# Kernel tuning notes

Hardware: AMD Instinct MI355X
Metric: run time of the kernel (lower is better)

The kernel has to match this reference:

```python
import jax, jax.numpy as jnp
import numpy as np

E = 2          # e_layers
DM = 64        # d_model == emb_dim (hardcoded 64 in out_layer)
H = 8          # n_heads
DH = DM // H
DFF = 256      # d_ff
P = 16         # patch_size
STRIDE = P // 2
SL = 4096      # seq_len
NPATCH = (SL - P) // STRIDE + 1   # 511
PRED = 96
B, M = 8, 8
FACTOR = 5
EPS = 1e-5


def setup_inputs() -> dict:
    key = jax.random.key(0)
    ks = jax.random.split(key, 32)
    s = jnp.float32(0.02)
    f = lambda i, shape: jax.random.normal(ks[i], shape, jnp.float32)
    d = {
        "x_enc": f(0, (B, SL, M)),
        "x_mark_enc": f(1, (B, SL, 4)),
        "x_dec": f(2, (B, PRED, M)),
        "x_mark_dec": f(3, (B, PRED, 4)),
        # patch embedding  Linear(patch_size -> emb_dim)
        "in_W": f(4, (DM, P)) * s,
        "in_b": jnp.zeros((DM,), jnp.float32),
        # per-layer attention projections (stacked over e_layers)
        "Wq": f(5, (E, DM, DM)) * s, "bq": jnp.zeros((E, DM), jnp.float32),
        "Wk": f(6, (E, DM, DM)) * s, "bk": jnp.zeros((E, DM), jnp.float32),
        "Wv": f(7, (E, DM, DM)) * s, "bv": jnp.zeros((E, DM), jnp.float32),
        "Wo": f(8, (E, DM, DM)) * s, "bo": jnp.zeros((E, DM), jnp.float32),
        # FFN (Conv1d kernel=1 == Linear)
        "c1_W": f(9, (E, DFF, DM)) * s, "c1_b": jnp.zeros((E, DFF), jnp.float32),
        "c2_W": f(10, (E, DM, DFF)) * s, "c2_b": jnp.zeros((E, DM), jnp.float32),
        # layer norms
        "ln1_g": jnp.ones((E, DM), jnp.float32), "ln1_b": jnp.zeros((E, DM), jnp.float32),
        "ln2_g": jnp.ones((E, DM), jnp.float32), "ln2_b": jnp.zeros((E, DM), jnp.float32),
        "lnf_g": jnp.ones((DM,), jnp.float32), "lnf_b": jnp.zeros((DM,), jnp.float32),
        # decode head  Linear(64*num_patches -> pred_len)
        "out_W": f(11, (PRED, DM * NPATCH)) * s,
        "out_b": jnp.zeros((PRED,), jnp.float32),
    }
    return d


def _ln(x, g, b):
    mu = x.mean(-1, keepdims=True)
    var = ((x - mu) ** 2).mean(-1, keepdims=True)
    return (x - mu) * jax.lax.rsqrt(var + EPS) * g + b


def _prob_attn(q, k, v, key):
    # q,k,v: [Bn, H, L, Dh]  (ProbSparse attention, mask_flag=False)
    Bn, h, Lq, Dh = q.shape
    Lk = k.shape[2]
    U_part = min(int(FACTOR * np.ceil(np.log(Lk))), Lk)   # sampled keys per query
    u = min(int(FACTOR * np.ceil(np.log(Lq))), Lq)        # top-u active queries
    idx = jax.random.randint(key, (Lq, U_part), 0, Lk)
    k_sample = k[:, :, idx, :]                             # [Bn,H,Lq,U,Dh]
    qk_sample = jnp.einsum('bhld,bhlud->bhlu', q, k_sample)
    # sparsity measure: max - sum/L_K (as in torch code)
    sparsity = qk_sample.max(-1) - qk_sample.sum(-1) / jnp.float32(Lk)
    _, top_idx = jax.lax.top_k(sparsity, u)                # [Bn,H,u]
    q_red = jnp.take_along_axis(q, top_idx[..., None], axis=2)  # [Bn,H,u,Dh]
    scale = jax.lax.rsqrt(jnp.float32(Dh))
    scores = jnp.einsum('bhud,bhkd->bhuk', q_red, k) * scale    # [Bn,H,u,Lk]
    attn = jax.nn.softmax(scores, axis=-1)
    # lazy context: mean of V for inactive queries, attn@V for active ones
    ctx = jnp.broadcast_to(v.mean(axis=2, keepdims=True), q.shape)
    upd = jnp.einsum('bhuk,bhkd->bhud', attn, v)
    bi = jnp.arange(Bn)[:, None, None]
    hi = jnp.arange(h)[None, :, None]
    ctx = ctx.at[bi, hi, top_idx].set(upd)
    return ctx.transpose(0, 2, 1, 3)  # [Bn,L,H,Dh]


def reference(x_enc, x_mark_enc, x_dec, x_mark_dec, in_W, in_b, Wq, bq, Wk, bk,
              Wv, bv, Wo, bo, c1_W, c1_b, c2_W, c2_b, ln1_g, ln1_b, ln2_g, ln2_b,
              lnf_g, lnf_b, out_W, out_b):
    Bb, L, Mm = x_enc.shape
    x = x_enc.transpose(0, 2, 1)  # b l m -> b m l
    pidx = jnp.arange(NPATCH)[:, None] * STRIDE + jnp.arange(P)[None, :]
    patches = x[:, :, pidx]                         # [B,M,N,P] (unfold)
    z = patches.reshape(Bb * Mm, NPATCH, P) @ in_W.T + in_b  # [BM,N,DM]
    akey = jax.random.key(1)
    for e in range(E):
        q = (z @ Wq[e].T + bq[e]).reshape(Bb * Mm, NPATCH, H, DH).transpose(0, 2, 1, 3)
        k = (z @ Wk[e].T + bk[e]).reshape(Bb * Mm, NPATCH, H, DH).transpose(0, 2, 1, 3)
        v = (z @ Wv[e].T + bv[e]).reshape(Bb * Mm, NPATCH, H, DH).transpose(0, 2, 1, 3)
        ctx = _prob_attn(q, k, v, jax.random.fold_in(akey, e))
        new_x = ctx.reshape(Bb * Mm, NPATCH, DM) @ Wo[e].T + bo[e]
        x1 = _ln(z + new_x, ln1_g[e], ln1_b[e])
        y = jax.nn.gelu(x1 @ c1_W[e].T + c1_b[e], approximate=False)
        y = y @ c2_W[e].T + c2_b[e]
        z = _ln(x1 + y, ln2_g[e], ln2_b[e])
    z = _ln(z, lnf_g, lnf_b)
    out = z.reshape(Bb * Mm, -1) @ out_W.T + out_b   # [BM, pred_len]
    out = out.reshape(Bb, Mm, PRED).transpose(0, 2, 1)  # (b m) l -> b l m
    return out[:, -PRED:, :]
```

## Files before the change

kernel.cpp:

```cpp
#include <hip/hip_runtime.h>
#include <hip/hip_bf16.h>
#include <stdint.h>
#include <math.h>

typedef __hip_bfloat16 bf16;
typedef __attribute__((ext_vector_type(8))) short short8;
typedef __attribute__((ext_vector_type(4))) short short4v;
typedef __attribute__((ext_vector_type(4))) float fx4;

#define NP 511
#define UPART 35
#define NTOK 32704
#define NBITS 17885
#define LN_EPS 1e-5f

__host__ __device__ __forceinline__ void tf2x32(uint32_t k0, uint32_t k1,
                                                uint32_t x0, uint32_t x1,
                                                uint32_t* o0, uint32_t* o1) {
  uint32_t ks2 = k0 ^ k1 ^ 0x1BD11BDAu;
  x0 += k0; x1 += k1;
#define TFR(r) { x0 += x1; x1 = (x1 << (r)) | (x1 >> (32 - (r))); x1 ^= x0; }
  TFR(13) TFR(15) TFR(26) TFR(6)   x0 += k1;  x1 += ks2 + 1u;
  TFR(17) TFR(29) TFR(16) TFR(24)  x0 += ks2; x1 += k0 + 2u;
  TFR(13) TFR(15) TFR(26) TFR(6)   x0 += k0;  x1 += k1 + 3u;
  TFR(17) TFR(29) TFR(16) TFR(24)  x0 += k1;  x1 += ks2 + 4u;
  TFR(13) TFR(15) TFR(26) TFR(6)   x0 += ks2; x1 += k0 + 5u;
#undef TFR
  *o0 = x0; *o1 = x1;
}

__device__ __forceinline__ float ldin(const void* p, int i, int f32) {
  if (f32) return ((const float*)p)[i];
  return __bfloat162float(((const bf16*)p)[i]);
}
__device__ __forceinline__ unsigned short f2bf(float v) {
  uint32_t u = __builtin_bit_cast(uint32_t, v);
  u += 0x7fffu + ((u >> 16) & 1u);
  return (unsigned short)(u >> 16);
}
__device__ __forceinline__ float bfb2f(uint32_t h) {
  uint32_t u = h << 16;
  return __builtin_bit_cast(float, u);
}
__device__ __forceinline__ float lo16(uint32_t w) { return bfb2f(w & 0xFFFFu); }
__device__ __forceinline__ float hi16(uint32_t w) { return bfb2f(w >> 16); }
__device__ __forceinline__ uint32_t pack2(float a, float b) {
  return (uint32_t)f2bf(a) | ((uint32_t)f2bf(b) << 16);
}
__device__ __forceinline__ int lanes_below(unsigned long long m) {
  return __builtin_amdgcn_mbcnt_hi((uint32_t)(m >> 32),
         __builtin_amdgcn_mbcnt_lo((uint32_t)m, 0));
}

__global__ void zero_out_kernel(bf16* __restrict__ out, int n) {
  int i = blockIdx.x * 256 + threadIdx.x;
  if (i < n) out[i] = __float2bfloat16(0.f);
}

__global__ void gen_idx_kernel(int* __restrict__ idxT,
    uint32_t ka0, uint32_t ka1, uint32_t kb0, uint32_t kb1,
    const uint32_t* __restrict__ lnfg, int* __restrict__ flag) {
  if (blockIdx.x == 0 && threadIdx.x == 0)
    flag[0] = (lnfg[0] == 0x3F800000u) ? 1 : 0;
  int i = blockIdx.x * 256 + threadIdx.x;
  if (i >= 2 * NBITS) return;
  int e = i / NBITS;
  uint32_t j = (uint32_t)(i - e * NBITS);
  uint32_t k0 = e ? kb0 : ka0, k1 = e ? kb1 : ka1;
  uint32_t o0, o1;
  tf2x32(k0, k1, 0u, j, &o0, &o1);
  uint32_t bits = o1;
  uint32_t hi = bits >> 16, lo = bits & 0xFFFFu;
  uint32_t off = ((hi % 511u) * 32u + (lo % 511u)) % 511u;
  int l = (int)(j / UPART), u = (int)(j % UPART);
  idxT[e * NBITS + u * NP + l] = (int)off;
}

__global__ __launch_bounds__(256) void embed_kernel(
    const void* __restrict__ xe, const void* __restrict__ inW,
    const void* __restrict__ inb, float* __restrict__ z,
    const int* __restrict__ flg) {
  __shared__ float xs[136 * 8];
  int f = flg[0];
  int b = blockIdx.x >> 5, nt = blockIdx.x & 31;
  int n0 = nt * 16;
  for (int i = threadIdx.x; i < 1088; i += 256) {
    int row = i >> 3, m = i & 7;
    int g = n0 * 8 + row;
    xs[i] = (g < 4096) ? ldin(xe, (b * 4096 + g) * 8 + m, f) : 0.f;
  }
  int d = threadIdx.x & 63, mg = threadIdx.x >> 6;
  float wreg[16];
#pragma unroll
  for (int p = 0; p < 16; ++p) wreg[p] = ldin(inW, d * 16 + p, f);
  float bd = ldin(inb, d, f);
  __syncthreads();
  for (int nl = 0; nl < 16; ++nl) {
    int n = n0 + nl;
    if (n >= NP) break;
#pragma unroll
    for (int mm = 0; mm < 2; ++mm) {
      int m = mg * 2 + mm;
      float acc = bd;
#pragma unroll
      for (int p = 0; p < 16; ++p)
        acc = fmaf(xs[(nl * 8 + p) * 8 + m], wreg[p], acc);
      int t = (b * 8 + m) * NP + n;
      z[(size_t)t * 64 + d] = acc;
    }
  }
}

__global__ __launch_bounds__(256) void qkv_kernel(
    const float* __restrict__ z,
    const void* __restrict__ Wq, const void* __restrict__ bq,
    const void* __restrict__ Wk, const void* __restrict__ bk,
    const void* __restrict__ Wv, const void* __restrict__ bv,
    bf16* __restrict__ qb, bf16* __restrict__ kb, bf16* __restrict__ vb,
    const int* __restrict__ flg, int e) {
  __shared__ short xb[64 * 72];
  __shared__ short wL[192 * 72];
  __shared__ float bqs[192];
  int f = flg[0];
  int t0 = blockIdx.x * 64;
  int tid = threadIdx.x;
  {
    const float4* xg = (const float4*)(z + (size_t)t0 * 64);
#pragma unroll
    for (int r = 0; r < 4; ++r) {
      int i4 = r * 256 + tid;
      float4 v = xg[i4];
      int t = (i4 * 4) >> 6, d = (i4 * 4) & 63;
      short4v h;
      h.x = (short)f2bf(v.x); h.y = (short)f2bf(v.y);
      h.z = (short)f2bf(v.z); h.w = (short)f2bf(v.w);
      *(short4v*)&xb[t * 72 + d] = h;
    }
  }
  if (!f) {
    const uint4* Wg0 = (const uint4*)((const bf16*)Wq + e * 4096);
    const uint4* Wg1 = (const uint4*)((const bf16*)Wk + e * 4096);
    const uint4* Wg2 = (const uint4*)((const bf16*)Wv + e * 4096);
#pragma unroll
    for (int r = 0; r < 2; ++r) {
      int i = r * 256 + tid;
      int row = i >> 3, c8 = (i & 7) * 8;
      *(uint4*)&wL[row * 72 + c8] = Wg0[i];
      *(uint4*)&wL[(64 + row) * 72 + c8] = Wg1[i];
      *(uint4*)&wL[(128 + row) * 72 + c8] = Wg2[i];
    }
  } else {
#pragma unroll
    for (int r = 0; r < 16; ++r) {
      int i = r * 256 + tid;
      int row = i >> 6, c = i & 63;
      wL[row * 72 + c] = (short)f2bf(((const float*)Wq)[e * 4096 + i]);
      wL[(64 + row) * 72 + c] = (short)f2bf(((const float*)Wk)[e * 4096 + i]);
      wL[(128 + row) * 72 + c] = (short)f2bf(((const float*)Wv)[e * 4096 + i]);
    }
  }
  if (tid < 192) {
    int t3 = tid >> 6, j = tid & 63;
    bqs[tid] = (t3 == 0) ? ldin(bq, e * 64 + j, f)
             : (t3 == 1) ? ldin(bk, e * 64 + j, f)
                         : ldin(bv, e * 64 + j, f);
  }
  __syncthreads();
  int lane = tid & 63, w = tid >> 6;
  int m0 = w * 16, col = lane & 15, quad = lane >> 4;
  short8 a0 = *(const short8*)&xb[(m0 + col) * 72 + quad * 8];
  short8 a1 = *(const short8*)&xb[(m0 + col) * 72 + 32 + quad * 8];
#pragma unroll
  for (int nt = 0; nt < 12; ++nt) {
    fx4 acc = {0.f, 0.f, 0.f, 0.f};
    short8 b0 = *(const short8*)&wL[(nt * 16 + col) * 72 + quad * 8];
    short8 b1 = *(const short8*)&wL[(nt * 16 + col) * 72 + 32 + quad * 8];
    acc = __builtin_amdgcn_mfma_f32_16x16x32_bf16(a0, b0, acc, 0, 0, 0);
    acc = __builtin_amdgcn_mfma_f32_16x16x32_bf16(a1, b1, acc, 0, 0, 0);
    int c = nt * 16 + col;
    int t3 = c >> 6, hd = c & 63, h = hd >> 3, d2 = hd & 7;
    bf16* base = (t3 == 0) ? qb : (t3 == 1) ? kb : vb;
    float bia = bqs[c];
#pragma unroll
    for (int reg = 0; reg < 4; ++reg) {
      int tok = t0 + m0 + quad * 4 + reg;
      int bm = tok / NP, n = tok - bm * NP;
      base[((size_t)(bm * 8 + h) * NP + n) * 8 + d2] =
          __float2bfloat16(acc[reg] + bia);
    }
  }
}

__global__ __launch_bounds__(512) void attn_fused_kernel(
    const bf16* __restrict__ qg, const bf16* __restrict__ kg,
    const bf16* __restrict__ vg, const int* __restrict__ idxT,
    bf16* __restrict__ ctx) {
  __shared__ uint32_t kkp[NP * 5 + 3];
  __shared__ uint32_t kvp[NP * 5 + 3];
  __shared__ float scF[8 * 512];
  __shared__ float spars[512];
  __shared__ float redv[256];
  __shared__ int topi[UPART];
  __shared__ float vmean[8];
  __shared__ unsigned char selflag[NP + 1];
  int bh = blockIdx.x;
  int bm = bh >> 3, h = bh & 7;
  size_t hb = (size_t)bh * NP * 8;
  int tid = threadIdx.x;
  int lane = tid & 63, wv = tid >> 6;
  {
    const uint4* k4 = (const uint4*)(kg + hb);
    const uint4* v4 = (const uint4*)(vg + hb);
    for (int n = tid; n < NP; n += 512) {
      uint4 b = k4[n], c = v4[n];
      uint32_t* dk = kkp + n * 5;
      uint32_t* dv = kvp + n * 5;
      dk[0] = b.x; dk[1] = b.y; dk[2] = b.z; dk[3] = b.w;
      dv[0] = c.x; dv[1] = c.y; dv[2] = c.z; dv[3] = c.w;
    }
  }
  __syncthreads();
  if (tid < NP) {
    int l = tid;
    uint4 a = ((const uint4*)(qg + hb))[l];
    float ql[8];
    ql[0] = lo16(a.x); ql[1] = hi16(a.x);
    ql[2] = lo16(a.y); ql[3] = hi16(a.y);
    ql[4] = lo16(a.z); ql[5] = hi16(a.z);
    ql[6] = lo16(a.w); ql[7] = hi16(a.w);
    float mxA = -1e30f, smA = 0.f, mxB = -1e30f, smB = 0.f;
#pragma unroll 6
    for (int u = 0; u < 18; ++u) {
      int j = idxT[u * NP + l];
      j = ((unsigned)j > 510u) ? 0 : j;
      const uint32_t* kr = kkp + j * 5;
      uint32_t w0 = kr[0], w1 = kr[1], w2 = kr[2], w3 = kr[3];
      float dt = 0.f;
      dt = fmaf(ql[0], lo16(w0), dt); dt = fmaf(ql[1], hi16(w0), dt);
      dt = fmaf(ql[2], lo16(w1), dt); dt = fmaf(ql[3], hi16(w1), dt);
      dt = fmaf(ql[4], lo16(w2), dt); dt = fmaf(ql[5], hi16(w2), dt);
      dt = fmaf(ql[6], lo16(w3), dt); dt = fmaf(ql[7], hi16(w3), dt);
      mxA = fmaxf(mxA, dt); smA += dt;
    }
#pragma unroll 6
    for (int u = 18; u < 35; ++u) {
      int j = idxT[u * NP + l];
      j = ((unsigned)j > 510u) ? 0 : j;
      const uint32_t* kr = kkp + j * 5;
      uint32_t w0 = kr[0], w1 = kr[1], w2 = kr[2], w3 = kr[3];
      float dt = 0.f;
      dt = fmaf(ql[0], lo16(w0), dt); dt = fmaf(ql[1], hi16(w0), dt);
      dt = fmaf(ql[2], lo16(w1), dt); dt = fmaf(ql[3], hi16(w1), dt);
      dt = fmaf(ql[4], lo16(w2), dt); dt = fmaf(ql[5], hi16(w2), dt);
      dt = fmaf(ql[6], lo16(w3), dt); dt = fmaf(ql[7], hi16(w3), dt);
      mxB = fmaxf(mxB, dt); smB += dt;
    }
    spars[l] = fmaxf(mxA, mxB) - (smA + smB) * (1.0f / 511.0f);
  }
  __syncthreads();
  if (tid < 64) {
    uint32_t key[8];
#pragma unroll
    for (int jj = 0; jj < 8; ++jj) {
      int ll = lane + jj * 64;
      if (ll < NP) {
        uint32_t u = __builtin_bit_cast(uint32_t, spars[ll]);
        key[jj] = (u & 0x80000000u) ? ~u : (u | 0x80000000u);
      } else key[jj] = 0u;
    }
    uint32_t p = 0u;
    for (int b = 31; b >= 0; --b) {
      uint32_t t = p | (1u << b);
      int cnt = 0;
#pragma unroll
      for (int jj = 0; jj < 8; ++jj)
        cnt += __popcll(__ballot(key[jj] >= t));
      if (cnt >= UPART) p = t;
    }
    int c1 = 0;
#pragma unroll
    for (int jj = 0; jj < 8; ++jj)
      c1 += __popcll(__ballot(key[jj] > p));
    int need = UPART - c1;
    int base = 0, taken = 0;
#pragma unroll
    for (int jj = 0; jj < 8; ++jj) {
      int ll = lane + jj * 64;
      bool gt = key[jj] > p;
      bool eq = key[jj] == p;
      unsigned long long meq = __ballot(eq);
      int beq = lanes_below(meq);
      bool sel = gt || (eq && (taken + beq) < need);
      unsigned long long msel = __ballot(sel);
      int pos = base + lanes_below(msel);
      if (sel) topi[pos] = ll;
      if (ll < NP) selflag[ll] = sel ? 1 : 0;
      base += __popcll(msel);
      taken += __popcll(meq);
    }
  } else if (tid >= 256) {
    int tt = tid - 256;
    int d = tt & 7, pt = tt >> 3;
    int c = d >> 1, odd = d & 1;
    float s = 0.f;
    for (int n = pt; n < NP; n += 32) {
      uint32_t w = kvp[n * 5 + c];
      s += odd ? hi16(w) : lo16(w);
    }
    redv[tt] = s;
  }
  __syncthreads();
  if (tid < 8) {
    float s = 0.f;
#pragma unroll
    for (int pt = 0; pt < 32; ++pt) s += redv[pt * 8 + tid];
    vmean[tid] = s * (1.0f / 511.0f);
  }
  __syncthreads();
  size_t cb = (size_t)bm * (NP * 64) + h * 8;
  if (tid < NP && !selflag[tid]) {
    uint4 pv;
    pv.x = pack2(vmean[0], vmean[1]);
    pv.y = pack2(vmean[2], vmean[3]);
    pv.z = pack2(vmean[4], vmean[5]);
    pv.w = pack2(vmean[6], vmean[7]);
    *(uint4*)(ctx + cb + (size_t)tid * 64) = pv;
  }
  const float scale = 0.35355339059327373f;
  float* myS = scF + wv * 512;
  int l0 = topi[wv];
  int l1 = topi[wv + 8];
  int l2 = topi[wv + 16];
  int l3 = topi[wv + 24];
  bool has5 = (wv + 32) < UPART;
  int l4 = has5 ? topi[wv + 32] : l0;
  l0 = ((unsigned)l0 > 510u) ? 0 : l0;
  l1 = ((unsigned)l1 > 510u) ? 0 : l1;
  l2 = ((unsigned)l2 > 510u) ? 0 : l2;
  l3 = ((unsigned)l3 > 510u) ? 0 : l3;
  l4 = ((unsigned)l4 > 510u) ? 0 : l4;
  const uint4* q4p = (const uint4*)(qg + hb);
  uint4 qv0 = q4p[l0];
  uint4 qv1 = q4p[l1];
  uint4 qv2 = q4p[l2];
  uint4 qv3 = q4p[l3];
  uint4 qv4 = q4p[l4];

  auto process = [&](uint4 a, int lsel) {
    float qs[8];
    qs[0] = lo16(a.x); qs[1] = hi16(a.x);
    qs[2] = lo16(a.y); qs[3] = hi16(a.y);
    qs[4] = lo16(a.z); qs[5] = hi16(a.z);
    qs[6] = lo16(a.w); qs[7] = hi16(a.w);
    float mx = -1e30f;
    for (int j = lane; j < NP; j += 64) {
      const uint32_t* kr = kkp + j * 5;
      uint32_t w0 = kr[0], w1 = kr[1], w2 = kr[2], w3 = kr[3];
      float d0 = qs[0] * lo16(w0);
      d0 = fmaf(qs[1], hi16(w0), d0);
      d0 = fmaf(qs[2], lo16(w1), d0);
      d0 = fmaf(qs[3], hi16(w1), d0);
      float d1 = qs[4] * lo16(w2);
      d1 = fmaf(qs[5], hi16(w2), d1);
      d1 = fmaf(qs[6], lo16(w3), d1);
      d1 = fmaf(qs[7], hi16(w3), d1);
      float sc = (d0 + d1) * scale;
      myS[j] = sc;
      mx = fmaxf(mx, sc);
    }
    for (int off = 32; off; off >>= 1) mx = fmaxf(mx, __shfl_xor(mx, off));
    float ssum = 0.f, acc[8];
#pragma unroll
    for (int d2 = 0; d2 < 8; ++d2) acc[d2] = 0.f;
    for (int j = lane; j < NP; j += 64) {
      float w = __expf(myS[j] - mx);
      ssum += w;
      const uint32_t* vr = kvp + j * 5;
      uint32_t x0 = vr[0], x1 = vr[1], x2 = vr[2], x3 = vr[3];
      acc[0] = fmaf(w, lo16(x0), acc[0]); acc[1] = fmaf(w, hi16(x0), acc[1]);
      acc[2] = fmaf(w, lo16(x1), acc[2]); acc[3] = fmaf(w, hi16(x1), acc[3]);
      acc[4] = fmaf(w, lo16(x2), acc[4]); acc[5] = fmaf(w, hi16(x2), acc[5]);
      acc[6] = fmaf(w, lo16(x3), acc[6]); acc[7] = fmaf(w, hi16(x3), acc[7]);
    }
    for (int off = 32; off; off >>= 1) {
      ssum += __shfl_xor(ssum, off);
#pragma unroll
      for (int d2 = 0; d2 < 8; ++d2) acc[d2] += __shfl_xor(acc[d2], off);
    }
    if (lane == 0) {
      float inv = 1.0f / ssum;
      uint4 pv;
      pv.x = pack2(acc[0] * inv, acc[1] * inv);
      pv.y = pack2(acc[2] * inv, acc[3] * inv);
      pv.z = pack2(acc[4] * inv, acc[5] * inv);
      pv.w = pack2(acc[6] * inv, acc[7] * inv);
      *(uint4*)(ctx + cb + (size_t)lsel * 64) = pv;
    }
  };
  process(qv0, l0);
  process(qv1, l1);
  process(qv2, l2);
  process(qv3, l3);
  if (has5) process(qv4, l4);
}

__global__ __launch_bounds__(256) void oproj_ln_kernel(
    const float* __restrict__ z, const bf16* __restrict__ ctx,
    const void* __restrict__ Wo, const void* __restrict__ bo,
    const void* __restrict__ g, const void* __restrict__ bb,
    float* __restrict__ x1, const int* __restrict__ flg, int e) {
  __shared__ short cbL[64 * 72];
  __shared__ short woL[64 * 72];
  __shared__ float zf[64 * 64];
  __shared__ float bos[64], gs[64], bbs[64];
  int f = flg[0];
  int t0 = blockIdx.x * 64;
  int tid = threadIdx.x;
  {
    const uint4* cg = (const uint4*)(ctx + (size_t)t0 * 64);
#pragma unroll
    for (int r = 0; r < 2; ++r) {
      int i = r * 256 + tid;
      uint4 v = cg[i];
      int row = i >> 3, c8 = (i & 7) * 8;
      *(uint4*)&cbL[row * 72 + c8] = v;
    }
    const float4* zg = (const float4*)(z + (size_t)t0 * 64);
#pragma unroll
    for (int r = 0; r < 4; ++r) {
      int i4 = r * 256 + tid;
      float4 v = zg[i4];
      int t = (i4 * 4) >> 6, d = (i4 * 4) & 63;
      *(float4*)&zf[t * 64 + d] = v;
    }
  }
  if (!f) {
    const uint4* Wg = (const uint4*)((const bf16*)Wo + e * 4096);
#pragma unroll
    for (int r = 0; r < 2; ++r) {
      int i = r * 256 + tid;
      int row = i >> 3, c8 = (i & 7) * 8;
      *(uint4*)&woL[row * 72 + c8] = Wg[i];
    }
  } else {
#pragma unroll
    for (int r = 0; r < 16; ++r) {
      int i = r * 256 + tid;
      int row = i >> 6, c = i & 63;
      woL[row * 72 + c] = (short)f2bf(((const float*)Wo)[e * 4096 + i]);
    }
  }
  if (tid < 64) {
    bos[tid] = ldin(bo, e * 64 + tid, f);
    gs[tid] = ldin(g, e * 64 + tid, f);
    bbs[tid] = ldin(bb, e * 64 + tid, f);
  }
  __syncthreads();
  int lane = tid & 63, w = tid >> 6;
  int m0 = w * 16, col = lane & 15, quad = lane >> 4;
  short8 a0 = *(const short8*)&cbL[(m0 + col) * 72 + quad * 8];
  short8 a1 = *(const short8*)&cbL[(m0 + col) * 72 + 32 + quad * 8];
  fx4 vacc[4];
#pragma unroll
  for (int nt = 0; nt < 4; ++nt) {
    fx4 acc = {0.f, 0.f, 0.f, 0.f};
    short8 b0 = *(const short8*)&woL[(nt * 16 + col) * 72 + quad * 8];
    short8 b1 = *(const short8*)&woL[(nt * 16 + col) * 72 + 32 + quad * 8];
    acc = __builtin_amdgcn_mfma_f32_16x16x32_bf16(a0, b0, acc, 0, 0, 0);
    acc = __builtin_amdgcn_mfma_f32_16x16x32_bf16(a1, b1, acc, 0, 0, 0);
    vacc[nt] = acc;
  }
  float vals[4][4];
  float ps[4], sq[4];
#pragma unroll
  for (int reg = 0; reg < 4; ++reg) { ps[reg] = 0.f; sq[reg] = 0.f; }
#pragma unroll
  for (int nt = 0; nt < 4; ++nt) {
    int d = nt * 16 + col;
#pragma unroll
    for (int reg = 0; reg < 4; ++reg) {
      int tl = m0 + quad * 4 + reg;
      float v = vacc[nt][reg] + bos[d] + zf[tl * 64 + d];
      vals[nt][reg] = v;
      ps[reg] += v; sq[reg] += v * v;
    }
  }
#pragma unroll
  for (int off = 1; off < 16; off <<= 1) {
#pragma unroll
    for (int reg = 0; reg < 4; ++reg) {
      ps[reg] += __shfl_xor(ps[reg], off);
      sq[reg] += __shfl_xor(sq[reg], off);
    }
  }
#pragma unroll
  for (int reg = 0; reg < 4; ++reg) {
    float mu = ps[reg] * (1.0f / 64.0f);
    float var = sq[reg] * (1.0f / 64.0f) - mu * mu;
    float rs = rsqrtf(fmaxf(var, 0.f) + LN_EPS);
    int tl = m0 + quad * 4 + reg;
#pragma unroll
    for (int nt = 0; nt < 4; ++nt) {
      int d = nt * 16 + col;
      x1[(size_t)(t0 + tl) * 64 + d] = (vals[nt][reg] - mu) * rs * gs[d] + bbs[d];
    }
  }
}

__global__ __launch_bounds__(256) void ffn_kernel(
    const float* __restrict__ x1,
    const void* __restrict__ W1, const void* __restrict__ b1,
    const void* __restrict__ W2, const void* __restrict__ b2,
    const void* __restrict__ g, const void* __restrict__ bb,
    float* __restrict__ zo, bf16* __restrict__ zfT,
    const void* __restrict__ lfg, const void* __restrict__ lfb,
    const int* __restrict__ flg, int e, int last) {
  __shared__ __align__(16) char smem[72960];
  short* wA  = (short*)smem;
  short* rB  = (short*)(smem + 36864);
  float* b1s = (float*)(smem + 70656);
  float* b2s = b1s + 256;
  float* gs  = b2s + 64;
  float* bbs = gs + 64;
  float* g2s = bbs + 64;
  float* bb2s = g2s + 64;
  int f = flg[0];
  int t0 = blockIdx.x * 64;
  int tid = threadIdx.x;
  {
    const float4* xg = (const float4*)(x1 + (size_t)t0 * 64);
#pragma unroll
    for (int r = 0; r < 4; ++r) {
      int i4 = r * 256 + tid;
      float4 v = xg[i4];
      int t = (i4 * 4) >> 6, d = (i4 * 4) & 63;
      short4v h;
      h.x = (short)f2bf(v.x); h.y = (short)f2bf(v.y);
      h.z = (short)f2bf(v.z); h.w = (short)f2bf(v.w);
      *(short4v*)&rB[t * 72 + d] = h;
    }
  }
  if (!f) {
    const uint4* W1g = (const uint4*)((const bf16*)W1 + e * 16384);
#pragma unroll
    for (int r = 0; r < 8; ++r) {
      int i = r * 256 + tid;
      uint4 v = W1g[i];
      int j = i >> 3, k = (i & 7) * 8;
      *(uint4*)&wA[j * 72 + k] = v;
    }
  } else {
    for (int r = 0; r < 64; ++r) {
      int i = r * 256 + tid;
      int j = i >> 6, k = i & 63;
      wA[j * 72 + k] = (short)f2bf(((const float*)W1)[e * 16384 + i]);
    }
  }
  b1s[tid] = ldin(b1, e * 256 + tid, f);
  if (tid < 64) {
    b2s[tid] = ldin(b2, e * 64 + tid, f);
    gs[tid] = ldin(g, e * 64 + tid, f);
    bbs[tid] = ldin(bb, e * 64 + tid, f);
    g2s[tid] = ldin(lfg, tid, f);
    bb2s[tid] = ldin(lfb, tid, f);
  }
  __syncthreads();

  int lane = tid & 63, w = tid >> 6;
  int m0 = w * 16;
  int col = lane & 15, quad = lane >> 4;
  short8 a0 = *(const short8*)&rB[(m0 + col) * 72 + quad * 8];
  short8 a1 = *(const short8*)&rB[(m0 + col) * 72 + 32 + quad * 8];
  __syncthreads();
#pragma unroll 4
  for (int nt = 0; nt < 16; ++nt) {
    fx4 acc = {0.f, 0.f, 0.f, 0.f};
    short8 bf0 = *(const short8*)&wA[(nt * 16 + col) * 72 + quad * 8];
    short8 bf1 = *(const short8*)&wA[(nt * 16 + col) * 72 + 32 + quad * 8];
    acc = __builtin_amdgcn_mfma_f32_16x16x32_bf16(a0, bf0, acc, 0, 0, 0);
    acc = __builtin_amdgcn_mfma_f32_16x16x32_bf16(a1, bf1, acc, 0, 0, 0);
    int j = nt * 16 + col;
    float bj = b1s[j];
#pragma unroll
    for (int reg = 0; reg < 4; ++reg) {
      float a = acc[reg] + bj;
      float ge = 0.5f * a * (1.0f + erff(a * 0.70710678118654752f));
      rB[(m0 + quad * 4 + reg) * 264 + j] = (short)f2bf(ge);
    }
  }
  __syncthreads();
  if (!f) {
    const uint4* W2g = (const uint4*)((const bf16*)W2 + e * 16384);
#pragma unroll
    for (int r = 0; r < 8; ++r) {
      int i = r * 256 + tid;
      uint4 v2 = W2g[i];
      int dd = i >> 5, c = (i & 31) * 8;
      *(uint4*)&wA[dd * 264 + c] = v2;
    }
  } else {
    for (int r = 0; r < 64; ++r) {
      int i = r * 256 + tid;
      int dd = i >> 8, c = i & 255;
      wA[dd * 264 + c] = (short)f2bf(((const float*)W2)[e * 16384 + i]);
    }
  }
  __syncthreads();
  short8 af[8];
#pragma unroll
  for (int kt = 0; kt < 8; ++kt)
    af[kt] = *(const short8*)&rB[(m0 + col) * 264 + kt * 32 + quad * 8];
  fx4 vacc[4];
#pragma unroll
  for (int nt = 0; nt < 4; ++nt) {
    fx4 acc = {0.f, 0.f, 0.f, 0.f};
#pragma unroll
    for (int kt = 0; kt < 8; ++kt) {
      short8 bfr = *(const short8*)&wA[(nt * 16 + col) * 264 + kt * 32 + quad * 8];
      acc = __builtin_amdgcn_mfma_f32_16x16x32_bf16(af[kt], bfr, acc, 0, 0, 0);
    }
    vacc[nt] = acc;
  }
  float vals[4][4];
  float ps[4], sq[4];
#pragma unroll
  for (int reg = 0; reg < 4; ++reg) { ps[reg] = 0.f; sq[reg] = 0.f; }
#pragma unroll
  for (int nt = 0; nt < 4; ++nt) {
    int d = nt * 16 + col;
#pragma unroll
    for (int reg = 0; reg < 4; ++reg) {
      int tl = m0 + quad * 4 + reg;
      float v = vacc[nt][reg] + b2s[d] + x1[(size_t)(t0 + tl) * 64 + d];
      vals[nt][reg] = v;
      ps[reg] += v; sq[reg] += v * v;
    }
  }
#pragma unroll
  for (int off = 1; off < 16; off <<= 1) {
#pragma unroll
    for (int reg = 0; reg < 4; ++reg) {
      ps[reg] += __shfl_xor(ps[reg], off);
      sq[reg] += __shfl_xor(sq[reg], off);
    }
  }
  if (!last) {
#pragma unroll
    for (int reg = 0; reg < 4; ++reg) {
      float mu = ps[reg] * (1.0f / 64.0f);
      float var = sq[reg] * (1.0f / 64.0f) - mu * mu;
      float rs = rsqrtf(fmaxf(var, 0.f) + LN_EPS);
      int tl = m0 + quad * 4 + reg;
#pragma unroll
      for (int nt = 0; nt < 4; ++nt) {
        int d = nt * 16 + col;
        zo[(size_t)(t0 + tl) * 64 + d] = (vals[nt][reg] - mu) * rs * gs[d] + bbs[d];
      }
    }
  } else {
    float ps2[4], sq2[4];
#pragma unroll
    for (int reg = 0; reg < 4; ++reg) { ps2[reg] = 0.f; sq2[reg] = 0.f; }
    float v2s[4][4];
#pragma unroll
    for (int reg = 0; reg < 4; ++reg) {
      float mu = ps[reg] * (1.0f / 64.0f);
      float var = sq[reg] * (1.0f / 64.0f) - mu * mu;
      float rs = rsqrtf(fmaxf(var, 0.f) + LN_EPS);
#pragma unroll
      for (int nt = 0; nt < 4; ++nt) {
        int d = nt * 16 + col;
        float v2 = (vals[nt][reg] - mu) * rs * gs[d] + bbs[d];
        v2s[nt][reg] = v2;
        ps2[reg] += v2; sq2[reg] += v2 * v2;
      }
    }
#pragma unroll
    for (int off = 1; off < 16; off <<= 1) {
#pragma unroll
      for (int reg = 0; reg < 4; ++reg) {
        ps2[reg] += __shfl_xor(ps2[reg], off);
        sq2[reg] += __shfl_xor(sq2[reg], off);
      }
    }
#pragma unroll
    for (int reg = 0; reg < 4; ++reg) {
      float mu = ps2[reg] * (1.0f / 64.0f);
      float var = sq2[reg] * (1.0f / 64.0f) - mu * mu;
      float rs = rsqrtf(fmaxf(var, 0.f) + LN_EPS);
      int tok = t0 + m0 + quad * 4 + reg;
      int bm = tok / NP, n = tok - bm * NP;
#pragma unroll
      for (int nt = 0; nt < 4; ++nt) {
        int d = nt * 16 + col;
        zfT[(size_t)n * 4096 + bm * 64 + d] =
            __float2bfloat16((v2s[nt][reg] - mu) * rs * g2s[d] + bb2s[d]);
      }
    }
  }
}

__global__ __launch_bounds__(256) void head1_kernel(
    const bf16* __restrict__ zfT, const void* __restrict__ W,
    float* __restrict__ partial, const int* __restrict__ flg) {
  __shared__ short aL[64 * 72];
  __shared__ short bL[96 * 72];
  int f = flg[0];
  int n = blockIdx.x;
  int tid = threadIdx.x;
  {
    const uint4* Ag = (const uint4*)(zfT + (size_t)n * 4096);
#pragma unroll
    for (int r = 0; r < 2; ++r) {
      int i = r * 256 + tid;
      uint4 v = Ag[i];
      int row = i >> 3, c = (i & 7) * 8;
      *(uint4*)&aL[row * 72 + c] = v;
    }
  }
  if (!f) {
    const uint4* Wg = (const uint4*)W;
#pragma unroll
    for (int r = 0; r < 3; ++r) {
      int i = r * 256 + tid;
      int p = i >> 3, c8 = i & 7;
      uint4 v = Wg[(size_t)p * 4088 + n * 8 + c8];
      *(uint4*)&bL[p * 72 + c8 * 8] = v;
    }
  } else {
    for (int r = 0; r < 24; ++r) {
      int i = r * 256 + tid;
      int p = i >> 6, c = i & 63;
      bL[p * 72 + c] = (short)f2bf(((const float*)W)[(size_t)p * 32704 + n * 64 + c]);
    }
  }
  __syncthreads();
  int lane = tid & 63, w = tid >> 6;
  int m0 = w * 16, col = lane & 15, quad = lane >> 4;
  short8 a0 = *(const short8*)&aL[(m0 + col) * 72 + quad * 8];
  short8 a1 = *(const short8*)&aL[(m0 + col) * 72 + 32 + quad * 8];
  float* pb = partial + (size_t)n * 6144;
#pragma unroll
  for (int nt = 0; nt < 6; ++nt) {
    fx4 acc = {0.f, 0.f, 0.f, 0.f};
    short8 b0 = *(const short8*)&bL[(nt * 16 + col) * 72 + quad * 8];
    short8 b1 = *(const short8*)&bL[(nt * 16 + col) * 72 + 32 + quad * 8];
    acc = __builtin_amdgcn_mfma_f32_16x16x32_bf16(a0, b0, acc, 0, 0, 0);
    acc = __builtin_amdgcn_mfma_f32_16x16x32_bf16(a1, b1, acc, 0, 0, 0);
#pragma unroll
    for (int reg = 0; reg < 4; ++reg)
      pb[(m0 + quad * 4 + reg) * 96 + nt * 16 + col] = acc[reg];
  }
}

__global__ __launch_bounds__(256) void head2_kernel(
    const float* __restrict__ partial, const void* __restrict__ bias,
    void* __restrict__ out, const int* __restrict__ flg) {
  __shared__ float red[4][64];
  int f = flg[0];
  int lane = threadIdx.x & 63, w = threadIdx.x >> 6;
  int j = blockIdx.x * 64 + lane;
  float acc = 0.f;
  for (int n = w; n < NP; n += 4)
    acc += partial[(size_t)n * 6144 + j];
  red[w][lane] = acc;
  __syncthreads();
  if (w == 0) {
    float s = red[0][lane] + red[1][lane] + red[2][lane] + red[3][lane];
    int bm = j / 96, p = j - bm * 96;
    float val = s + ldin(bias, p, f);
    int b = bm >> 3, m = bm & 7;
    int o = (b * 96 + p) * 8 + m;
    if (f) ((float*)out)[o] = val;
    else   ((bf16*)out)[o] = __float2bfloat16(val);
  }
}

extern "C" void kernel_launch(void* const* d_in, const int* in_sizes, int n_in,
                              void* d_out, int out_size, void* d_ws, size_t ws_size,
                              hipStream_t stream) {
  const void* xe  = d_in[0];
  const void* inW = d_in[4];
  const void* inb = d_in[5];
  const void* Wq  = d_in[6];
  const void* bq  = d_in[7];
  const void* Wk  = d_in[8];
  const void* bk  = d_in[9];
  const void* Wv  = d_in[10];
  const void* bv  = d_in[11];
  const void* Wo  = d_in[12];
  const void* bo  = d_in[13];
  const void* c1W = d_in[14];
  const void* c1b = d_in[15];
  const void* c2W = d_in[16];
  const void* c2b = d_in[17];
  const void* l1g = d_in[18];
  const void* l1b = d_in[19];
  const void* l2g = d_in[20];
  const void* l2b = d_in[21];
  const void* lfg = d_in[22];
  const void* lfb = d_in[23];
  const void* oW  = d_in[24];
  const void* obv = d_in[25];

  const size_t NF = (size_t)NTOK * 64;
  const size_t REQ = (3 * NF + 2 * NBITS + 32) * sizeof(float);
  if (ws_size < REQ) {
    zero_out_kernel<<<(out_size + 255) / 256, 256, 0, stream>>>((bf16*)d_out, out_size);
    return;
  }

  float* z   = (float*)d_ws;
  bf16* ctxb = (bf16*)(z + NF);
  bf16* qb   = (bf16*)(z + NF + NF / 2);
  bf16* kb   = (bf16*)(z + 2 * NF);
  bf16* vb   = (bf16*)(z + 2 * NF + NF / 2);
  float* x1  = z + 2 * NF;
  int* idxb  = (int*)(z + 3 * NF);
  int* flg   = idxb + 2 * NBITS;
  bf16* zfT  = ctxb;
  float* partial = z;

  uint32_t ke[2][2];
  for (int e = 0; e < 2; ++e)
    tf2x32(0u, 1u, 0u, (uint32_t)e, &ke[e][0], &ke[e][1]);
  gen_idx_kernel<<<(2 * NBITS + 255) / 256, 256, 0, stream>>>(idxb,
      ke[0][0], ke[0][1], ke[1][0], ke[1][1], (const uint32_t*)lfg, flg);

  embed_kernel<<<256, 256, 0, stream>>>(xe, inW, inb, z, flg);
  for (int e = 0; e < 2; ++e) {
    qkv_kernel<<<NTOK / 64, 256, 0, stream>>>(z, Wq, bq, Wk, bk, Wv, bv,
        qb, kb, vb, flg, e);
    attn_fused_kernel<<<512, 512, 0, stream>>>(qb, kb, vb, idxb + e * NBITS,
        ctxb);
    oproj_ln_kernel<<<NTOK / 64, 256, 0, stream>>>(z, ctxb, Wo, bo, l1g, l1b,
        x1, flg, e);
    ffn_kernel<<<NTOK / 64, 256, 0, stream>>>(x1, c1W, c1b, c2W, c2b,
        l2g, l2b, z, zfT, lfg, lfb, flg, e, e == 1);
  }
  head1_kernel<<<NP, 256, 0, stream>>>(zfT, oW, partial, flg);
  head2_kernel<<<96, 256, 0, stream>>>(partial, obv, d_out, flg);
}
```

Before: 317.7 us.

## Double attention block threads, split sparsity sampling and keep scores in registers

The fused ProbSparse attention kernel now launches 1024 threads per block instead of 512. K and V staging is split between the two thread halves, the 35 sampled-key loop is split into two halves combined through shared memory, and the V-mean reduction is moved to overlap with the combine step. With 16 waves each handles up to three top queries instead of five. The per-wave score buffer in shared memory is replaced by an unrolled 8-element register array, which lowers LDS use at the cost of register pressure under the 1024-thread launch bound.

```diff
diff --git a/kernel.cpp b/kernel.cpp
--- a/kernel.cpp
+++ b/kernel.cpp
@@ -191,14 +191,14 @@
   }
 }
 
-__global__ __launch_bounds__(512) void attn_fused_kernel(
+__global__ __launch_bounds__(1024, 8) void attn_fused_kernel(
     const bf16* __restrict__ qg, const bf16* __restrict__ kg,
     const bf16* __restrict__ vg, const int* __restrict__ idxT,
     bf16* __restrict__ ctx) {
-  __shared__ uint32_t kkp[NP * 5 + 3];
-  __shared__ uint32_t kvp[NP * 5 + 3];
-  __shared__ float scF[8 * 512];
+  __shared__ uint32_t kkp[NP * 5 + 5];
+  __shared__ uint32_t kvp[NP * 5 + 5];
   __shared__ float spars[512];
+  __shared__ float mxB_s[512], smB_s[512];
   __shared__ float redv[256];
   __shared__ int topi[UPART];
   __shared__ float vmean[8];
@@ -208,18 +208,22 @@
   size_t hb = (size_t)bh * NP * 8;
   int tid = threadIdx.x;
   int lane = tid & 63, wv = tid >> 6;
-  {
-    const uint4* k4 = (const uint4*)(kg + hb);
-    const uint4* v4 = (const uint4*)(vg + hb);
-    for (int n = tid; n < NP; n += 512) {
-      uint4 b = k4[n], c = v4[n];
-      uint32_t* dk = kkp + n * 5;
+  if (tid < 512) {
+    if (tid < NP) {
+      uint4 b = ((const uint4*)(kg + hb))[tid];
+      uint32_t* dk = kkp + tid * 5;
+      dk[0] = b.x; dk[1] = b.y; dk[2] = b.z; dk[3] = b.w;
+    }
+  } else {
+    int n = tid - 512;
+    if (n < NP) {
+      uint4 c = ((const uint4*)(vg + hb))[n];
       uint32_t* dv = kvp + n * 5;
-      dk[0] = b.x; dk[1] = b.y; dk[2] = b.z; dk[3] = b.w;
       dv[0] = c.x; dv[1] = c.y; dv[2] = c.z; dv[3] = c.w;
     }
   }
   __syncthreads();
+  float mxA = -1e30f, smA = 0.f;
   if (tid < NP) {
     int l = tid;
     uint4 a = ((const uint4*)(qg + hb))[l];
@@ -228,7 +232,6 @@
     ql[2] = lo16(a.y); ql[3] = hi16(a.y);
     ql[4] = lo16(a.z); ql[5] = hi16(a.z);
     ql[6] = lo16(a.w); ql[7] = hi16(a.w);
-    float mxA = -1e30f, smA = 0.f, mxB = -1e30f, smB = 0.f;
 #pragma unroll 6
     for (int u = 0; u < 18; ++u) {
       int j = idxT[u * NP + l];
@@ -242,6 +245,15 @@
       dt = fmaf(ql[6], lo16(w3), dt); dt = fmaf(ql[7], hi16(w3), dt);
       mxA = fmaxf(mxA, dt); smA += dt;
     }
+  } else if (tid >= 512 && tid < 512 + NP) {
+    int l = tid - 512;
+    uint4 a = ((const uint4*)(qg + hb))[l];
+    float ql[8];
+    ql[0] = lo16(a.x); ql[1] = hi16(a.x);
+    ql[2] = lo16(a.y); ql[3] = hi16(a.y);
+    ql[4] = lo16(a.z); ql[5] = hi16(a.z);
+    ql[6] = lo16(a.w); ql[7] = hi16(a.w);
+    float mxB = -1e30f, smB = 0.f;
 #pragma unroll 6
     for (int u = 18; u < 35; ++u) {
       int j = idxT[u * NP + l];
@@ -255,7 +267,21 @@
       dt = fmaf(ql[6], lo16(w3), dt); dt = fmaf(ql[7], hi16(w3), dt);
       mxB = fmaxf(mxB, dt); smB += dt;
     }
-    spars[l] = fmaxf(mxA, mxB) - (smA + smB) * (1.0f / 511.0f);
+    mxB_s[l] = mxB; smB_s[l] = smB;
+  }
+  __syncthreads();
+  if (tid < NP) {
+    spars[tid] = fmaxf(mxA, mxB_s[tid]) - (smA + smB_s[tid]) * (1.0f / 511.0f);
+  } else if (tid >= 512 && tid < 768) {
+    int tt = tid - 512;
+    int d = tt & 7, pt = tt >> 3;
+    int c = d >> 1, odd = d & 1;
+    float s = 0.f;
+    for (int n = pt; n < NP; n += 32) {
+      uint32_t w = kvp[n * 5 + c];
+      s += odd ? hi16(w) : lo16(w);
+    }
+    redv[tt] = s;
   }
   __syncthreads();
   if (tid < 64) {
@@ -298,23 +324,12 @@
       base += __popcll(msel);
       taken += __popcll(meq);
     }
-  } else if (tid >= 256) {
-    int tt = tid - 256;
-    int d = tt & 7, pt = tt >> 3;
-    int c = d >> 1, odd = d & 1;
+  } else if (tid >= 64 && tid < 72) {
+    int d = tid - 64;
     float s = 0.f;
-    for (int n = pt; n < NP; n += 32) {
-      uint32_t w = kvp[n * 5 + c];
-      s += odd ? hi16(w) : lo16(w);
-    }
-    redv[tt] = s;
-  }
-  __syncthreads();
-  if (tid < 8) {
-    float s = 0.f;
-#pragma unroll
-    for (int pt = 0; pt < 32; ++pt) s += redv[pt * 8 + tid];
-    vmean[tid] = s * (1.0f / 511.0f);
+#pragma unroll
+    for (int pt = 0; pt < 32; ++pt) s += redv[pt * 8 + d];
+    vmean[d] = s * (1.0f / 511.0f);
   }
   __syncthreads();
   size_t cb = (size_t)bm * (NP * 64) + h * 8;
@@ -327,24 +342,17 @@
     *(uint4*)(ctx + cb + (size_t)tid * 64) = pv;
   }
   const float scale = 0.35355339059327373f;
-  float* myS = scF + wv * 512;
   int l0 = topi[wv];
-  int l1 = topi[wv + 8];
-  int l2 = topi[wv + 16];
-  int l3 = topi[wv + 24];
-  bool has5 = (wv + 32) < UPART;
-  int l4 = has5 ? topi[wv + 32] : l0;
+  int l1 = topi[wv + 16];
+  bool has3 = (wv + 32) < UPART;
+  int l2 = has3 ? topi[wv + 32] : l0;
   l0 = ((unsigned)l0 > 510u) ? 0 : l0;
   l1 = ((unsigned)l1 > 510u) ? 0 : l1;
   l2 = ((unsigned)l2 > 510u) ? 0 : l2;
-  l3 = ((unsigned)l3 > 510u) ? 0 : l3;
-  l4 = ((unsigned)l4 > 510u) ? 0 : l4;
   const uint4* q4p = (const uint4*)(qg + hb);
   uint4 qv0 = q4p[l0];
   uint4 qv1 = q4p[l1];
   uint4 qv2 = q4p[l2];
-  uint4 qv3 = q4p[l3];
-  uint4 qv4 = q4p[l4];
 
   auto process = [&](uint4 a, int lsel) {
     float qs[8];
@@ -352,9 +360,13 @@
     qs[2] = lo16(a.y); qs[3] = hi16(a.y);
     qs[4] = lo16(a.z); qs[5] = hi16(a.z);
     qs[6] = lo16(a.w); qs[7] = hi16(a.w);
+    float sreg[8];
     float mx = -1e30f;
-    for (int j = lane; j < NP; j += 64) {
-      const uint32_t* kr = kkp + j * 5;
+#pragma unroll
+    for (int s = 0; s < 8; ++s) {
+      int j = lane + s * 64;
+      int jc = (j > 510) ? 0 : j;
+      const uint32_t* kr = kkp + jc * 5;
       uint32_t w0 = kr[0], w1 = kr[1], w2 = kr[2], w3 = kr[3];
       float d0 = qs[0] * lo16(w0);
       d0 = fmaf(qs[1], hi16(w0), d0);
@@ -365,17 +377,20 @@
       d1 = fmaf(qs[6], lo16(w3), d1);
       d1 = fmaf(qs[7], hi16(w3), d1);
       float sc = (d0 + d1) * scale;
-      myS[j] = sc;
-      mx = fmaxf(mx, sc);
+      sreg[s] = (j > 510) ? -1e30f : sc;
+      mx = fmaxf(mx, sreg[s]);
     }
     for (int off = 32; off; off >>= 1) mx = fmaxf(mx, __shfl_xor(mx, off));
     float ssum = 0.f, acc[8];
 #pragma unroll
     for (int d2 = 0; d2 < 8; ++d2) acc[d2] = 0.f;
-    for (int j = lane; j < NP; j += 64) {
-      float w = __expf(myS[j] - mx);
+#pragma unroll
+    for (int s = 0; s < 8; ++s) {
+      int j = lane + s * 64;
+      int jc = (j > 510) ? 0 : j;
+      float w = __expf(sreg[s] - mx);
       ssum += w;
-      const uint32_t* vr = kvp + j * 5;
+      const uint32_t* vr = kvp + jc * 5;
       uint32_t x0 = vr[0], x1 = vr[1], x2 = vr[2], x3 = vr[3];
       acc[0] = fmaf(w, lo16(x0), acc[0]); acc[1] = fmaf(w, hi16(x0), acc[1]);
       acc[2] = fmaf(w, lo16(x1), acc[2]); acc[3] = fmaf(w, hi16(x1), acc[3]);
@@ -399,9 +414,7 @@
   };
   process(qv0, l0);
   process(qv1, l1);
-  process(qv2, l2);
-  process(qv3, l3);
-  if (has5) process(qv4, l4);
+  if (has3) process(qv2, l2);
 }
 
 __global__ __launch_bounds__(256) void oproj_ln_kernel(
@@ -831,7 +844,7 @@
   for (int e = 0; e < 2; ++e) {
     qkv_kernel<<<NTOK / 64, 256, 0, stream>>>(z, Wq, bq, Wk, bk, Wv, bv,
         qb, kb, vb, flg, e);
-    attn_fused_kernel<<<512, 512, 0, stream>>>(qb, kb, vb, idxb + e * NBITS,
+    attn_fused_kernel<<<512, 1024, 0, stream>>>(qb, kb, vb, idxb + e * NBITS,
         ctxb);
     oproj_ln_kernel<<<NTOK / 64, 256, 0, stream>>>(z, ctxb, Wo, bo, l1g, l1b,
         x1, flg, e);
```

Result: no change. 311.8 us (-1.9%).
